# Kernel tuning notes

Measured on AMD Instinct MI355X. Metric: run time of the kernel, lower is better.

The kernel has to match this reference:

```python
import jax, jax.numpy as jnp
import numpy as np

LOOKBACK = 512
T = 131072
FEES = 0.00025


def setup_inputs() -> dict:
    key = jax.random.key(0)
    k1, k2, k3, k4 = jax.random.split(key, 4)
    features = jax.random.normal(k1, (T,), dtype=jnp.float32)
    # gross per-step asset returns near 1.0 (hourly price relatives)
    asset_returns = 1.0 + 0.01 * jax.random.normal(k2, (T,), dtype=jnp.float32)
    theta = jax.random.uniform(k3, (LOOKBACK + 2,), dtype=jnp.float32)  # torch.rand init
    p_init = jax.random.uniform(k4, (LOOKBACK - 1,), dtype=jnp.float32)  # the lookback-1 seed positions
    return {"features": features, "asset_returns": asset_returns, "theta": theta, "p_init": p_init}


def _positions(features, theta, p_init):
    lb = theta.shape[0] - 2
    n_steps = features.shape[0] - lb + 1
    # all sliding windows features[t-lb:t], t = lb..T  -> [n_steps, lb]
    idx = jnp.arange(n_steps)[:, None] + jnp.arange(lb)[None, :]
    win = features[idx]
    wmean = win.mean(axis=1, keepdims=True)
    wstd = jnp.std(win, axis=1, ddof=1, keepdims=True)  # torch.std is unbiased
    win_norm = (win - wmean) / wstd

    # running stats over ALL positions so far (growing list in the original)
    n0 = jnp.asarray(p_init.shape[0], dtype=jnp.float32)
    state0 = (n0, p_init.sum(), jnp.sum(p_init * p_init), p_init[-1])

    one = jnp.ones((1,), dtype=features.dtype)

    def step(state, w):
        n, s, ss, p_last = state
        mean = s / n
        std = jnp.sqrt((ss - n * mean * mean) / (n - 1.0))
        last_norm = (p_last - mean) / std
        xt = jnp.concatenate([w, last_norm[None], one])  # [lb+2]
        xt = (xt - xt.mean()) / jnp.std(xt, ddof=1)
        p_new = jax.nn.sigmoid(jnp.dot(theta, xt))
        return (n + 1.0, s + p_new, ss + p_new * p_new, p_new), p_new

    _, p_seq = jax.lax.scan(step, state0, win_norm)
    return jnp.concatenate([p_init, p_seq])  # length T


def _bot_returns(P, asset_returns, fees):
    inv0 = P[0]
    cash0 = 1.0 - inv0

    def step(state, rp):
        inv, cash = state
        r, p = rp
        inv = inv * r
        pv = inv + cash
        delta = pv * p - inv  # desired - current investment
        inv = inv + jnp.where(delta > 0, delta * (1.0 - fees), delta)
        cash = cash + jnp.where(delta > 0, -delta, -delta * (1.0 - fees))
        return (inv, cash), inv + cash

    _, pv_tail = jax.lax.scan(step, (inv0, cash0), (asset_returns[1:], P[1:]))
    pv = jnp.concatenate([jnp.ones((1,), dtype=pv_tail.dtype), pv_tail])  # length T
    ratios = pv[1:] / pv[:-1]
    return jnp.concatenate([jnp.ones((1,), dtype=ratios.dtype), ratios])


def reference(features, asset_returns, theta, p_init):
    P = _positions(features, theta, p_init)
    return _bot_returns(P, asset_returns, FEES)
```

## Files before the change

### kernel.cpp

```cpp
#include <hip/hip_runtime.h>
#include <math.h>

#define T_TOTAL 131072
#define LB      512
#define NSTEPS  130561
#define NPAD    130564
#define OMF     0.99975f
#define KC     -1.4426950408889634f

#define OFF_E    0
#define OFF_P0   (NPAD)
#define OFF_P    (2*NPAD)
#define OFF_BS   (2*NPAD + T_TOTAL)
#define OFF_BSS  (OFF_BS + 1024)
#define OFF_CP   (OFF_BSS + 1024)

static __device__ __forceinline__ float fast_rcp(float x) {
#if __has_builtin(__builtin_amdgcn_rcpf)
    return __builtin_amdgcn_rcpf(x);
#else
    return 1.0f / x;
#endif
}
static __device__ __forceinline__ float fast_rsq(float x) {
#if __has_builtin(__builtin_amdgcn_rsqf)
    return __builtin_amdgcn_rsqf(x);
#else
    return 1.0f / sqrtf(x);
#endif
}
static __device__ __forceinline__ float fast_exp2(float x) {
#if __has_builtin(__builtin_amdgcn_exp2f)
    return __builtin_amdgcn_exp2f(x);
#else
    return exp2f(x);
#endif
}

__global__ __launch_bounds__(256) void precompute_kernel(
    const float* __restrict__ features,
    const float* __restrict__ theta,
    const float* __restrict__ p_init,
    float* __restrict__ e_out,
    float* __restrict__ p0_out,
    float* __restrict__ P,
    float* __restrict__ bs,
    float* __restrict__ bss,
    float* __restrict__ cpool)
{
    __shared__ float f_lds[1536];
    __shared__ float th_lds[512];
    const int tid = threadIdx.x;
    const int b   = blockIdx.x;
    const int base = b * 1024;

    {
        const float4* fg = (const float4*)features;
        float4* f4s = (float4*)f_lds;
        int g0 = b * 256 + tid; g0 = g0 > 32767 ? 32767 : g0;
        f4s[tid] = fg[g0];
        if (tid < 128) {
            int g1 = b * 256 + 256 + tid; g1 = g1 > 32767 ? 32767 : g1;
            f4s[256 + tid] = fg[g1];
        }
        const float4* tg = (const float4*)theta;
        float4* t4s = (float4*)th_lds;
        if (tid >= 128 && tid < 256) t4s[tid - 128] = tg[tid - 128];
    }
    if (b == 0) {
        P[tid] = p_init[tid < 511 ? tid : 510];
        if (tid + 256 < 511) P[tid + 256] = p_init[tid + 256];
    }
    __syncthreads();

    const float4* f4 = (const float4*)f_lds;
    const float4* t4 = (const float4*)th_lds;

    float d0 = 0.f, d1 = 0.f, d2 = 0.f, d3 = 0.f;
    float fsum0 = 0.f, fss0 = 0.f, thsum = 0.f;
    float4 a = f4[tid];
    const float a00 = a.x, a01 = a.y, a02 = a.z;
#pragma unroll 4
    for (int j = 0; j < 128; ++j) {
        float4 bb = f4[tid + j + 1];
        float4 th = t4[j];
        thsum += (th.x + th.y) + (th.z + th.w);
        d0 = fmaf(th.x, a.x, d0); d0 = fmaf(th.y, a.y, d0);
        d0 = fmaf(th.z, a.z, d0); d0 = fmaf(th.w, a.w, d0);
        d1 = fmaf(th.x, a.y, d1); d1 = fmaf(th.y, a.z, d1);
        d1 = fmaf(th.z, a.w, d1); d1 = fmaf(th.w, bb.x, d1);
        d2 = fmaf(th.x, a.z, d2); d2 = fmaf(th.y, a.w, d2);
        d2 = fmaf(th.z, bb.x, d2); d2 = fmaf(th.w, bb.y, d2);
        d3 = fmaf(th.x, a.w, d3); d3 = fmaf(th.y, bb.x, d3);
        d3 = fmaf(th.z, bb.y, d3); d3 = fmaf(th.w, bb.z, d3);
        fsum0 += (a.x + a.y) + (a.z + a.w);
        fss0 = fmaf(a.x, a.x, fss0); fss0 = fmaf(a.y, a.y, fss0);
        fss0 = fmaf(a.z, a.z, fss0); fss0 = fmaf(a.w, a.w, fss0);
        a = bb;
    }
    const float b00 = a.x, b01 = a.y, b02 = a.z;
    const float fsum1 = fsum0 - a00 + b00;
    const float fsum2 = fsum1 - a01 + b01;
    const float fsum3 = fsum2 - a02 + b02;
    float fss1 = fss0 - a00 * a00; fss1 = fmaf(b00, b00, fss1);
    float fss2 = fss1 - a01 * a01; fss2 = fmaf(b01, b01, fss2);
    float fss3 = fss2 - a02 * a02; fss3 = fmaf(b02, b02, fss3);

    const float th512 = theta[512];
    const float th513 = theta[513];
    const float sall  = thsum + th512 + th513;
    const float A_    = (512.0f - 1.0f / 514.0f) / 513.0f;
    const float rsqA  = fast_rsq(A_);
    const float cE    = th513 - sall * (1.0f / 514.0f);
    if (b == 0 && tid == 0) cpool[0] = KC * (th512 - sall * (1.0f / 514.0f));

    float ez[4], pv[4];
    const float fs_[4]  = { fsum0, fsum1, fsum2, fsum3 };
    const float fq_[4]  = { fss0,  fss1,  fss2,  fss3  };
    const float dd_[4]  = { d0, d1, d2, d3 };
#pragma unroll
    for (int c = 0; c < 4; ++c) {
        float m    = fs_[c] * (1.0f / 512.0f);
        float varw = (fq_[c] - fs_[c] * m) * (1.0f / 511.0f);
        float dn   = (dd_[c] - m * thsum) * fast_rsq(varw);
        float E    = dn + cE;
        ez[c] = KC * E;
        pv[c] = fast_rcp(1.0f + fast_exp2(ez[c] * rsqA));
    }

    const int t4i = base + 4 * tid;
    if (t4i + 3 < NSTEPS) {
        ((float4*)e_out)[b * 256 + tid]  = make_float4(ez[0], ez[1], ez[2], ez[3]);
        ((float4*)p0_out)[b * 256 + tid] = make_float4(pv[0], pv[1], pv[2], pv[3]);
    } else {
#pragma unroll
        for (int c = 0; c < 4; ++c)
            if (t4i + c < NSTEPS) { e_out[t4i + c] = ez[c]; p0_out[t4i + c] = pv[c]; }
    }

    float c1 = 0.f, c2 = 0.f;
#pragma unroll
    for (int c = 0; c < 4; ++c) {
        float p = (t4i + c < NSTEPS) ? pv[c] : 0.f;
        c1 += p; c2 = fmaf(p, p, c2);
    }
#pragma unroll
    for (int dlt = 16; dlt; dlt >>= 1) {
        c1 += __shfl_down(c1, dlt, 64);
        c2 += __shfl_down(c2, dlt, 64);
    }
    if ((tid & 31) == 0) {
        int idx = b * 8 + (tid >> 5);
        bs[idx] = c1; bss[idx] = c2;
    }
}

__global__ __launch_bounds__(64) void pos_kernel(
    const float* __restrict__ p_init,
    const float* __restrict__ e,
    const float* __restrict__ p0,
    const float* __restrict__ bs,
    const float* __restrict__ bss,
    const float* __restrict__ cpool,
    float* __restrict__ P)
{
    const int l = threadIdx.x;
    const int b = blockIdx.x;
    const int g = b * 64 + l;

    float sa = 0.f, qa = 0.f;
    for (int j = l; j < 511; j += 64) { float v = p_init[j]; sa += v; qa = fmaf(v, v, qa); }
#pragma unroll
    for (int dlt = 32; dlt; dlt >>= 1) { sa += __shfl_xor(sa, dlt, 64); qa += __shfl_xor(qa, dlt, 64); }

    float ba = 0.f, ca = 0.f;
    for (int j = l; j < b * 64; j += 64) { ba += bs[j]; ca += bss[j]; }
#pragma unroll
    for (int dlt = 32; dlt; dlt >>= 1) { ba += __shfl_xor(ba, dlt, 64); ca += __shfl_xor(ca, dlt, 64); }

    float vb = (g < 1021) ? bs[g] : 0.f;
    float vc = (g < 1021) ? bss[g] : 0.f;
    float ib = vb, ic = vc;
#pragma unroll
    for (int dlt = 1; dlt < 64; dlt <<= 1) {
        float ub = __shfl_up(ib, dlt, 64);
        float uc = __shfl_up(ic, dlt, 64);
        if (l >= dlt) { ib += ub; ic += uc; }
    }
    float s  = sa + ba + (ib - vb);
    float ss = qa + ca + (ic - vc);

    if (g >= 1021) return;

    const float Gp = cpool[0];
    const float A_ = (512.0f - 1.0f / 514.0f) / 513.0f;
    const float B_ = (1.0f - 1.0f / 514.0f) / 513.0f;
    const float C_ = -2.0f / (514.0f * 513.0f);

    const int k0   = g * 128;
    const int kend = (k0 + 128 < NSTEPS) ? k0 + 128 : NSTEPS;
    const int kw   = (g == 0) ? 0 : k0 - 16;

    float plast = (g == 0) ? p_init[510] : p0[k0 - 17];
    float nf    = 511.0f + (float)k0;
    float rnm1  = fast_rcp(nf - 1.0f);

    const float mean_f = s * fast_rcp(nf);
    const float rv_f   = fast_rsq(fmaf(-s, mean_f, ss) * rnm1);

    const float4* e4 = (const float4*)(e + kw);
    const int maxi = (NPAD / 4 - 1) - (kw >> 2);

    float4 eb0[4], eb1[4];
#define LDB(DST, T) { \
    int i0 = 4 * (T); \
    DST[0] = e4[(i0 + 0) < maxi ? (i0 + 0) : maxi]; \
    DST[1] = e4[(i0 + 1) < maxi ? (i0 + 1) : maxi]; \
    DST[2] = e4[(i0 + 2) < maxi ? (i0 + 2) : maxi]; \
    DST[3] = e4[(i0 + 3) < maxi ? (i0 + 3) : maxi]; }

#define STEPF(EK, I) { \
    float rn   = fast_rcp(nf); \
    float mean = s * rn; \
    float varp = fmaf(-s, mean, ss) * rnm1; \
    float rv   = fast_rsq(varp); \
    float u    = (plast - mean) * rv; \
    float vx   = fmaf(u, fmaf(B_, u, C_), A_); \
    float r2   = fast_rsq(vx); \
    float z    = fmaf(u, Gp, (EK)) * r2; \
    float w    = fast_exp2(z); \
    float pnew = fast_rcp(1.0f + w); \
    s += pnew; ss = fmaf(pnew, pnew, ss); plast = pnew; \
    rnm1 = rn; nf += 1.0f; \
    int k = kw + (I); \
    if (k < kend) P[511 + k] = pnew; }

#define STEPW(EK) { \
    float u    = (plast - mean_f) * rv_f; \
    float vx   = fmaf(u, fmaf(B_, u, C_), A_); \
    float r2   = fast_rsq(vx); \
    float z    = fmaf(u, Gp, (EK)) * r2; \
    float w    = fast_exp2(z); \
    plast = fast_rcp(1.0f + w); }

#define FULLB(EB, IB) { \
    STEPF(EB[0].x, IB + 0);  STEPF(EB[0].y, IB + 1);  STEPF(EB[0].z, IB + 2);  STEPF(EB[0].w, IB + 3); \
    STEPF(EB[1].x, IB + 4);  STEPF(EB[1].y, IB + 5);  STEPF(EB[1].z, IB + 6);  STEPF(EB[1].w, IB + 7); \
    STEPF(EB[2].x, IB + 8);  STEPF(EB[2].y, IB + 9);  STEPF(EB[2].z, IB + 10); STEPF(EB[2].w, IB + 11); \
    STEPF(EB[3].x, IB + 12); STEPF(EB[3].y, IB + 13); STEPF(EB[3].z, IB + 14); STEPF(EB[3].w, IB + 15); }

#define WARMB(EB) { \
    STEPW(EB[0].x); STEPW(EB[0].y); STEPW(EB[0].z); STEPW(EB[0].w); \
    STEPW(EB[1].x); STEPW(EB[1].y); STEPW(EB[1].z); STEPW(EB[1].w); \
    STEPW(EB[2].x); STEPW(EB[2].y); STEPW(EB[2].z); STEPW(EB[2].w); \
    STEPW(EB[3].x); STEPW(EB[3].y); STEPW(EB[3].z); STEPW(EB[3].w); }

    LDB(eb0, 0); LDB(eb1, 1);
    if (g == 0) { FULLB(eb0, 0); } else { WARMB(eb0); }
    LDB(eb0, 2); FULLB(eb1, 16);
    LDB(eb1, 3); FULLB(eb0, 32);
    LDB(eb0, 4); FULLB(eb1, 48);
    LDB(eb1, 5); FULLB(eb0, 64);
    LDB(eb0, 6); FULLB(eb1, 80);
    LDB(eb1, 7); FULLB(eb0, 96);
    LDB(eb0, 8); FULLB(eb1, 112);
    FULLB(eb0, 128);
#undef LDB
#undef STEPF
#undef STEPW
#undef FULLB
#undef WARMB
}

__global__ __launch_bounds__(64) void port_kernel(
    const float* __restrict__ ar,
    const float* __restrict__ Pp,
    float* __restrict__ out)
{
    const int l = threadIdx.x;
    const int b = blockIdx.x;
    const int g = b * 64 + l;

    const int t0   = (g == 0) ? 1 : g * 64;
    const int tend = (t0 + 64 < T_TOTAL) ? t0 + 64 : T_TOTAL;
    const int tw   = (g == 0) ? 0 : t0 - 16;

    float x = Pp[(g == 0) ? 0 : (tw - 1)];
    float inv = x, cash = 1.0f - x, pvprev = 1.0f;
    if (g == 0) out[0] = 1.0f;

    const float4* P4 = (const float4*)(Pp + tw);
    const float4* A4 = (const float4*)(ar + tw);

    float4 pb0[4], ab0[4], pb1[4], ab1[4];
#define LDC(PD, AD, T) { \
    int i0 = 4 * (T); \
    PD[0] = P4[i0 + 0]; PD[1] = P4[i0 + 1]; PD[2] = P4[i0 + 2]; PD[3] = P4[i0 + 3]; \
    AD[0] = A4[i0 + 0]; AD[1] = A4[i0 + 1]; AD[2] = A4[i0 + 2]; AD[3] = A4[i0 + 3]; }

#define CSTEP(RR, PPV, I) { \
    int t = tw + (I); \
    float invn  = inv * (RR); \
    float pv    = invn + cash; \
    float delta = fmaf(pv, (PPV), -invn); \
    float dfee  = delta * OMF; \
    bool  pos   = delta > 0.0f; \
    float inv2  = invn + (pos ? dfee : delta); \
    float cash2 = cash - (pos ? delta : dfee); \
    float pvn   = inv2 + cash2; \
    if (t >= 1) { \
        if (t >= t0 && t < tend) out[t] = pvn * fast_rcp(pvprev); \
        inv = inv2; cash = cash2; pvprev = pvn; \
    } }

#define CBATCH(PB, AB, IB) { \
    CSTEP(AB[0].x, PB[0].x, IB + 0);  CSTEP(AB[0].y, PB[0].y, IB + 1); \
    CSTEP(AB[0].z, PB[0].z, IB + 2);  CSTEP(AB[0].w, PB[0].w, IB + 3); \
    CSTEP(AB[1].x, PB[1].x, IB + 4);  CSTEP(AB[1].y, PB[1].y, IB + 5); \
    CSTEP(AB[1].z, PB[1].z, IB + 6);  CSTEP(AB[1].w, PB[1].w, IB + 7); \
    CSTEP(AB[2].x, PB[2].x, IB + 8);  CSTEP(AB[2].y, PB[2].y, IB + 9); \
    CSTEP(AB[2].z, PB[2].z, IB + 10); CSTEP(AB[2].w, PB[2].w, IB + 11); \
    CSTEP(AB[3].x, PB[3].x, IB + 12); CSTEP(AB[3].y, PB[3].y, IB + 13); \
    CSTEP(AB[3].z, PB[3].z, IB + 14); CSTEP(AB[3].w, PB[3].w, IB + 15); }

    LDC(pb0, ab0, 0); LDC(pb1, ab1, 1);
    CBATCH(pb0, ab0, 0);  LDC(pb0, ab0, 2);
    CBATCH(pb1, ab1, 16); LDC(pb1, ab1, 3);
    CBATCH(pb0, ab0, 32); LDC(pb0, ab0, 4);
    CBATCH(pb1, ab1, 48);
    CBATCH(pb0, ab0, 64);
#undef LDC
#undef CSTEP
#undef CBATCH
}

extern "C" void kernel_launch(void* const* d_in, const int* in_sizes, int n_in,
                              void* d_out, int out_size, void* d_ws, size_t ws_size,
                              hipStream_t stream) {
    const float* features      = (const float*)d_in[0];
    const float* asset_returns = (const float*)d_in[1];
    const float* theta         = (const float*)d_in[2];
    const float* p_init        = (const float*)d_in[3];
    float* out = (float*)d_out;
    float* ws  = (float*)d_ws;

    float* e_arr = ws + OFF_E;
    float* p0    = ws + OFF_P0;
    float* P     = ws + OFF_P;
    float* bs    = ws + OFF_BS;
    float* bss   = ws + OFF_BSS;
    float* cpool = ws + OFF_CP;

    precompute_kernel<<<128, 256, 0, stream>>>(features, theta, p_init,
                                               e_arr, p0, P, bs, bss, cpool);
    pos_kernel<<<16, 64, 0, stream>>>(p_init, e_arr, p0, bs, bss, cpool, P);
    port_kernel<<<32, 64, 0, stream>>>(asset_returns, P, out);
}
```

Baseline: 99.43 us.

## Fuse three kernels into one persistent kernel with grid barriers, halve chunk sizes

Merges the precompute, position-scan and portfolio-scan kernels into one 128-block launch separated by atomic-counter grid barriers, plus a tiny init kernel that zeroes the counters. This removes two kernel-launch gaps. The sequential chunks are halved (64-step position chunks with 8-step warm-up, 32-step portfolio chunks with 8-step warm-up), so more threads run shorter serial chains. Partial sums are now taken per 16 lanes to match the smaller chunks. The costs are barrier spin overhead, an extra launch for the counter reset, and shorter warm-up windows that could reduce accuracy.

```diff
diff --git a/kernel.cpp b/kernel.cpp
--- a/kernel.cpp
+++ b/kernel.cpp
@@ -12,8 +12,9 @@
 #define OFF_P0   (NPAD)
 #define OFF_P    (2*NPAD)
 #define OFF_BS   (2*NPAD + T_TOTAL)
-#define OFF_BSS  (OFF_BS + 1024)
-#define OFF_CP   (OFF_BSS + 1024)
+#define OFF_BSS  (OFF_BS + 2048)
+#define OFF_CP   (OFF_BSS + 2048)
+#define OFF_CTR  (OFF_CP + 16)
 
 static __device__ __forceinline__ float fast_rcp(float x) {
 #if __has_builtin(__builtin_amdgcn_rcpf)
@@ -37,189 +38,205 @@
 #endif
 }
 
-__global__ __launch_bounds__(256) void precompute_kernel(
+static __device__ __forceinline__ void grid_barrier(unsigned* ctr, unsigned nblk) {
+    __syncthreads();
+    if (threadIdx.x == 0) {
+        __threadfence();
+        __hip_atomic_fetch_add(ctr, 1u, __ATOMIC_ACQ_REL, __HIP_MEMORY_SCOPE_AGENT);
+        while (__hip_atomic_load(ctr, __ATOMIC_ACQUIRE, __HIP_MEMORY_SCOPE_AGENT) < nblk) {
+            __builtin_amdgcn_s_sleep(8);
+        }
+        __threadfence();
+    }
+    __syncthreads();
+}
+
+__global__ __launch_bounds__(64) void init_kernel(unsigned* ctr) {
+    ctr[threadIdx.x] = 0u;
+}
+
+__global__ __launch_bounds__(256) void fused_kernel(
     const float* __restrict__ features,
+    const float* __restrict__ asset_returns,
     const float* __restrict__ theta,
     const float* __restrict__ p_init,
-    float* __restrict__ e_out,
-    float* __restrict__ p0_out,
-    float* __restrict__ P,
-    float* __restrict__ bs,
-    float* __restrict__ bss,
-    float* __restrict__ cpool)
+    float* __restrict__ out,
+    float* __restrict__ ws)
 {
+    float* e_out = ws + OFF_E;
+    float* p0    = ws + OFF_P0;
+    float* P     = ws + OFF_P;
+    float* bs    = ws + OFF_BS;
+    float* bss   = ws + OFF_BSS;
+    float* cpool = ws + OFF_CP;
+    unsigned* ctr = (unsigned*)(ws + OFF_CTR);
+
     __shared__ float f_lds[1536];
     __shared__ float th_lds[512];
     const int tid = threadIdx.x;
     const int b   = blockIdx.x;
-    const int base = b * 1024;
 
     {
-        const float4* fg = (const float4*)features;
-        float4* f4s = (float4*)f_lds;
-        int g0 = b * 256 + tid; g0 = g0 > 32767 ? 32767 : g0;
-        f4s[tid] = fg[g0];
-        if (tid < 128) {
-            int g1 = b * 256 + 256 + tid; g1 = g1 > 32767 ? 32767 : g1;
-            f4s[256 + tid] = fg[g1];
-        }
-        const float4* tg = (const float4*)theta;
-        float4* t4s = (float4*)th_lds;
-        if (tid >= 128 && tid < 256) t4s[tid - 128] = tg[tid - 128];
+        const int base = b * 1024;
+        {
+            const float4* fg = (const float4*)features;
+            float4* f4s = (float4*)f_lds;
+            int g0 = b * 256 + tid; g0 = g0 > 32767 ? 32767 : g0;
+            f4s[tid] = fg[g0];
+            if (tid < 128) {
+                int g1 = b * 256 + 256 + tid; g1 = g1 > 32767 ? 32767 : g1;
+                f4s[256 + tid] = fg[g1];
+            }
+            const float4* tg = (const float4*)theta;
+            float4* t4s = (float4*)th_lds;
+            if (tid >= 128 && tid < 256) t4s[tid - 128] = tg[tid - 128];
+        }
+        if (b == 0) {
+            P[tid] = p_init[tid < 511 ? tid : 510];
+            if (tid + 256 < 511) P[tid + 256] = p_init[tid + 256];
+        }
+        __syncthreads();
+
+        float thsum = 0.f;
+        {
+            int l6 = tid & 63;
+#pragma unroll
+            for (int j = 0; j < 8; ++j) thsum += th_lds[l6 + 64 * j];
+#pragma unroll
+            for (int d = 32; d; d >>= 1) thsum += __shfl_xor(thsum, d, 64);
+        }
+
+        const float4* f4 = (const float4*)f_lds;
+        const float4* t4 = (const float4*)th_lds;
+
+        float d0 = 0.f, d1 = 0.f, d2 = 0.f, d3 = 0.f;
+        float fsum0 = 0.f, fss0 = 0.f;
+        float4 a = f4[tid];
+        const float a00 = a.x, a01 = a.y, a02 = a.z;
+#pragma unroll 4
+        for (int j = 0; j < 128; ++j) {
+            float4 bb = f4[tid + j + 1];
+            float4 th = t4[j];
+            d0 = fmaf(th.x, a.x, d0); d0 = fmaf(th.y, a.y, d0);
+            d0 = fmaf(th.z, a.z, d0); d0 = fmaf(th.w, a.w, d0);
+            d1 = fmaf(th.x, a.y, d1); d1 = fmaf(th.y, a.z, d1);
+            d1 = fmaf(th.z, a.w, d1); d1 = fmaf(th.w, bb.x, d1);
+            d2 = fmaf(th.x, a.z, d2); d2 = fmaf(th.y, a.w, d2);
+            d2 = fmaf(th.z, bb.x, d2); d2 = fmaf(th.w, bb.y, d2);
+            d3 = fmaf(th.x, a.w, d3); d3 = fmaf(th.y, bb.x, d3);
+            d3 = fmaf(th.z, bb.y, d3); d3 = fmaf(th.w, bb.z, d3);
+            fsum0 += (a.x + a.y) + (a.z + a.w);
+            fss0 = fmaf(a.x, a.x, fss0); fss0 = fmaf(a.y, a.y, fss0);
+            fss0 = fmaf(a.z, a.z, fss0); fss0 = fmaf(a.w, a.w, fss0);
+            a = bb;
+        }
+        const float b00 = a.x, b01 = a.y, b02 = a.z;
+        const float fsum1 = fsum0 - a00 + b00;
+        const float fsum2 = fsum1 - a01 + b01;
+        const float fsum3 = fsum2 - a02 + b02;
+        float fss1 = fss0 - a00 * a00; fss1 = fmaf(b00, b00, fss1);
+        float fss2 = fss1 - a01 * a01; fss2 = fmaf(b01, b01, fss2);
+        float fss3 = fss2 - a02 * a02; fss3 = fmaf(b02, b02, fss3);
+
+        const float th512 = theta[512];
+        const float th513 = theta[513];
+        const float sall  = thsum + th512 + th513;
+        const float A_    = (512.0f - 1.0f / 514.0f) / 513.0f;
+        const float rsqA  = fast_rsq(A_);
+        const float cE    = th513 - sall * (1.0f / 514.0f);
+        if (b == 0 && tid == 0) cpool[0] = KC * (th512 - sall * (1.0f / 514.0f));
+
+        float ez[4], pv[4];
+        const float fs_[4] = { fsum0, fsum1, fsum2, fsum3 };
+        const float fq_[4] = { fss0,  fss1,  fss2,  fss3  };
+        const float dd_[4] = { d0, d1, d2, d3 };
+#pragma unroll
+        for (int c = 0; c < 4; ++c) {
+            float m    = fs_[c] * (1.0f / 512.0f);
+            float varw = (fq_[c] - fs_[c] * m) * (1.0f / 511.0f);
+            float dn   = (dd_[c] - m * thsum) * fast_rsq(varw);
+            ez[c] = KC * (dn + cE);
+            pv[c] = fast_rcp(1.0f + fast_exp2(ez[c] * rsqA));
+        }
+
+        const int t4i = base + 4 * tid;
+        if (t4i + 3 < NSTEPS) {
+            ((float4*)e_out)[b * 256 + tid] = make_float4(ez[0], ez[1], ez[2], ez[3]);
+            ((float4*)p0)[b * 256 + tid]    = make_float4(pv[0], pv[1], pv[2], pv[3]);
+        } else {
+#pragma unroll
+            for (int c = 0; c < 4; ++c)
+                if (t4i + c < NSTEPS) { e_out[t4i + c] = ez[c]; p0[t4i + c] = pv[c]; }
+        }
+
+        float c1 = 0.f, c2 = 0.f;
+#pragma unroll
+        for (int c = 0; c < 4; ++c) {
+            float p = (t4i + c < NSTEPS) ? pv[c] : 0.f;
+            c1 += p; c2 = fmaf(p, p, c2);
+        }
+#pragma unroll
+        for (int d = 8; d; d >>= 1) {
+            c1 += __shfl_down(c1, d, 16);
+            c2 += __shfl_down(c2, d, 16);
+        }
+        if ((tid & 15) == 0) {
+            int idx = b * 16 + (tid >> 4);
+            bs[idx] = c1; bss[idx] = c2;
+        }
     }
-    if (b == 0) {
-        P[tid] = p_init[tid < 511 ? tid : 510];
-        if (tid + 256 < 511) P[tid + 256] = p_init[tid + 256];
-    }
-    __syncthreads();
-
-    const float4* f4 = (const float4*)f_lds;
-    const float4* t4 = (const float4*)th_lds;
-
-    float d0 = 0.f, d1 = 0.f, d2 = 0.f, d3 = 0.f;
-    float fsum0 = 0.f, fss0 = 0.f, thsum = 0.f;
-    float4 a = f4[tid];
-    const float a00 = a.x, a01 = a.y, a02 = a.z;
-#pragma unroll 4
-    for (int j = 0; j < 128; ++j) {
-        float4 bb = f4[tid + j + 1];
-        float4 th = t4[j];
-        thsum += (th.x + th.y) + (th.z + th.w);
-        d0 = fmaf(th.x, a.x, d0); d0 = fmaf(th.y, a.y, d0);
-        d0 = fmaf(th.z, a.z, d0); d0 = fmaf(th.w, a.w, d0);
-        d1 = fmaf(th.x, a.y, d1); d1 = fmaf(th.y, a.z, d1);
-        d1 = fmaf(th.z, a.w, d1); d1 = fmaf(th.w, bb.x, d1);
-        d2 = fmaf(th.x, a.z, d2); d2 = fmaf(th.y, a.w, d2);
-        d2 = fmaf(th.z, bb.x, d2); d2 = fmaf(th.w, bb.y, d2);
-        d3 = fmaf(th.x, a.w, d3); d3 = fmaf(th.y, bb.x, d3);
-        d3 = fmaf(th.z, bb.y, d3); d3 = fmaf(th.w, bb.z, d3);
-        fsum0 += (a.x + a.y) + (a.z + a.w);
-        fss0 = fmaf(a.x, a.x, fss0); fss0 = fmaf(a.y, a.y, fss0);
-        fss0 = fmaf(a.z, a.z, fss0); fss0 = fmaf(a.w, a.w, fss0);
-        a = bb;
-    }
-    const float b00 = a.x, b01 = a.y, b02 = a.z;
-    const float fsum1 = fsum0 - a00 + b00;
-    const float fsum2 = fsum1 - a01 + b01;
-    const float fsum3 = fsum2 - a02 + b02;
-    float fss1 = fss0 - a00 * a00; fss1 = fmaf(b00, b00, fss1);
-    float fss2 = fss1 - a01 * a01; fss2 = fmaf(b01, b01, fss2);
-    float fss3 = fss2 - a02 * a02; fss3 = fmaf(b02, b02, fss3);
-
-    const float th512 = theta[512];
-    const float th513 = theta[513];
-    const float sall  = thsum + th512 + th513;
-    const float A_    = (512.0f - 1.0f / 514.0f) / 513.0f;
-    const float rsqA  = fast_rsq(A_);
-    const float cE    = th513 - sall * (1.0f / 514.0f);
-    if (b == 0 && tid == 0) cpool[0] = KC * (th512 - sall * (1.0f / 514.0f));
-
-    float ez[4], pv[4];
-    const float fs_[4]  = { fsum0, fsum1, fsum2, fsum3 };
-    const float fq_[4]  = { fss0,  fss1,  fss2,  fss3  };
-    const float dd_[4]  = { d0, d1, d2, d3 };
-#pragma unroll
-    for (int c = 0; c < 4; ++c) {
-        float m    = fs_[c] * (1.0f / 512.0f);
-        float varw = (fq_[c] - fs_[c] * m) * (1.0f / 511.0f);
-        float dn   = (dd_[c] - m * thsum) * fast_rsq(varw);
-        float E    = dn + cE;
-        ez[c] = KC * E;
-        pv[c] = fast_rcp(1.0f + fast_exp2(ez[c] * rsqA));
-    }
-
-    const int t4i = base + 4 * tid;
-    if (t4i + 3 < NSTEPS) {
-        ((float4*)e_out)[b * 256 + tid]  = make_float4(ez[0], ez[1], ez[2], ez[3]);
-        ((float4*)p0_out)[b * 256 + tid] = make_float4(pv[0], pv[1], pv[2], pv[3]);
-    } else {
-#pragma unroll
-        for (int c = 0; c < 4; ++c)
-            if (t4i + c < NSTEPS) { e_out[t4i + c] = ez[c]; p0_out[t4i + c] = pv[c]; }
-    }
-
-    float c1 = 0.f, c2 = 0.f;
-#pragma unroll
-    for (int c = 0; c < 4; ++c) {
-        float p = (t4i + c < NSTEPS) ? pv[c] : 0.f;
-        c1 += p; c2 = fmaf(p, p, c2);
-    }
-#pragma unroll
-    for (int dlt = 16; dlt; dlt >>= 1) {
-        c1 += __shfl_down(c1, dlt, 64);
-        c2 += __shfl_down(c2, dlt, 64);
-    }
-    if ((tid & 31) == 0) {
-        int idx = b * 8 + (tid >> 5);
-        bs[idx] = c1; bss[idx] = c2;
-    }
-}
-
-__global__ __launch_bounds__(64) void pos_kernel(
-    const float* __restrict__ p_init,
-    const float* __restrict__ e,
-    const float* __restrict__ p0,
-    const float* __restrict__ bs,
-    const float* __restrict__ bss,
-    const float* __restrict__ cpool,
-    float* __restrict__ P)
-{
-    const int l = threadIdx.x;
-    const int b = blockIdx.x;
-    const int g = b * 64 + l;
-
-    float sa = 0.f, qa = 0.f;
-    for (int j = l; j < 511; j += 64) { float v = p_init[j]; sa += v; qa = fmaf(v, v, qa); }
-#pragma unroll
-    for (int dlt = 32; dlt; dlt >>= 1) { sa += __shfl_xor(sa, dlt, 64); qa += __shfl_xor(qa, dlt, 64); }
-
-    float ba = 0.f, ca = 0.f;
-    for (int j = l; j < b * 64; j += 64) { ba += bs[j]; ca += bss[j]; }
-#pragma unroll
-    for (int dlt = 32; dlt; dlt >>= 1) { ba += __shfl_xor(ba, dlt, 64); ca += __shfl_xor(ca, dlt, 64); }
-
-    float vb = (g < 1021) ? bs[g] : 0.f;
-    float vc = (g < 1021) ? bss[g] : 0.f;
-    float ib = vb, ic = vc;
-#pragma unroll
-    for (int dlt = 1; dlt < 64; dlt <<= 1) {
-        float ub = __shfl_up(ib, dlt, 64);
-        float uc = __shfl_up(ic, dlt, 64);
-        if (l >= dlt) { ib += ub; ic += uc; }
-    }
-    float s  = sa + ba + (ib - vb);
-    float ss = qa + ca + (ic - vc);
-
-    if (g >= 1021) return;
-
-    const float Gp = cpool[0];
-    const float A_ = (512.0f - 1.0f / 514.0f) / 513.0f;
-    const float B_ = (1.0f - 1.0f / 514.0f) / 513.0f;
-    const float C_ = -2.0f / (514.0f * 513.0f);
-
-    const int k0   = g * 128;
-    const int kend = (k0 + 128 < NSTEPS) ? k0 + 128 : NSTEPS;
-    const int kw   = (g == 0) ? 0 : k0 - 16;
-
-    float plast = (g == 0) ? p_init[510] : p0[k0 - 17];
-    float nf    = 511.0f + (float)k0;
-    float rnm1  = fast_rcp(nf - 1.0f);
-
-    const float mean_f = s * fast_rcp(nf);
-    const float rv_f   = fast_rsq(fmaf(-s, mean_f, ss) * rnm1);
-
-    const float4* e4 = (const float4*)(e + kw);
-    const int maxi = (NPAD / 4 - 1) - (kw >> 2);
-
-    float4 eb0[4], eb1[4];
-#define LDB(DST, T) { \
-    int i0 = 4 * (T); \
-    DST[0] = e4[(i0 + 0) < maxi ? (i0 + 0) : maxi]; \
-    DST[1] = e4[(i0 + 1) < maxi ? (i0 + 1) : maxi]; \
-    DST[2] = e4[(i0 + 2) < maxi ? (i0 + 2) : maxi]; \
-    DST[3] = e4[(i0 + 3) < maxi ? (i0 + 3) : maxi]; }
-
-#define STEPF(EK, I) { \
+
+    grid_barrier(&ctr[0], 128);
+
+    if (b < 32 && tid < 64) {
+        const int l = tid;
+        const int g = b * 64 + l;
+
+        float sa = 0.f, qa = 0.f;
+        for (int j = l; j < 511; j += 64) { float v = p_init[j]; sa += v; qa = fmaf(v, v, qa); }
+#pragma unroll
+        for (int d = 32; d; d >>= 1) { sa += __shfl_xor(sa, d, 64); qa += __shfl_xor(qa, d, 64); }
+
+        float ba = 0.f, ca = 0.f;
+        for (int j = l; j < b * 64; j += 64) { ba += bs[j]; ca += bss[j]; }
+#pragma unroll
+        for (int d = 32; d; d >>= 1) { ba += __shfl_xor(ba, d, 64); ca += __shfl_xor(ca, d, 64); }
+
+        float vb = bs[g], vc = bss[g];
+        float ib = vb, ic = vc;
+#pragma unroll
+        for (int d = 1; d < 64; d <<= 1) {
+            float ub = __shfl_up(ib, d, 64);
+            float uc = __shfl_up(ic, d, 64);
+            if (l >= d) { ib += ub; ic += uc; }
+        }
+        float s  = sa + ba + (ib - vb);
+        float ss = qa + ca + (ic - vc);
+
+        if (g <= 2040) {
+            const float Gp = cpool[0];
+            const float A_ = (512.0f - 1.0f / 514.0f) / 513.0f;
+            const float B_ = (1.0f - 1.0f / 514.0f) / 513.0f;
+            const float C_ = -2.0f / (514.0f * 513.0f);
+
+            const int k0   = g * 64;
+            const int kend = (k0 + 64 < NSTEPS) ? k0 + 64 : NSTEPS;
+            const int kw   = (g == 0) ? 0 : k0 - 8;
+
+            float plast = (g == 0) ? p_init[510] : p0[k0 - 9];
+            float nf    = 511.0f + (float)k0;
+            float rnm1  = fast_rcp(nf - 1.0f);
+            const float mean_f = s * fast_rcp(nf);
+            const float rv_f   = fast_rsq(fmaf(-s, mean_f, ss) * rnm1);
+
+            const float4* e4 = (const float4*)(e_out + kw);
+            const int maxi = (NPAD / 4 - 1) - (kw >> 2);
+
+            float4 er[18];
+#pragma unroll
+            for (int i = 0; i < 18; ++i) er[i] = e4[i < maxi ? i : maxi];
+
+#define BSTEP(EK, I) { \
     float rn   = fast_rcp(nf); \
     float mean = s * rn; \
     float varp = fmaf(-s, mean, ss) * rnm1; \
@@ -234,104 +251,72 @@
     rnm1 = rn; nf += 1.0f; \
     int k = kw + (I); \
     if (k < kend) P[511 + k] = pnew; }
-
-#define STEPW(EK) { \
-    float u    = (plast - mean_f) * rv_f; \
-    float vx   = fmaf(u, fmaf(B_, u, C_), A_); \
-    float r2   = fast_rsq(vx); \
-    float z    = fmaf(u, Gp, (EK)) * r2; \
-    float w    = fast_exp2(z); \
-    plast = fast_rcp(1.0f + w); }
-
-#define FULLB(EB, IB) { \
-    STEPF(EB[0].x, IB + 0);  STEPF(EB[0].y, IB + 1);  STEPF(EB[0].z, IB + 2);  STEPF(EB[0].w, IB + 3); \
-    STEPF(EB[1].x, IB + 4);  STEPF(EB[1].y, IB + 5);  STEPF(EB[1].z, IB + 6);  STEPF(EB[1].w, IB + 7); \
-    STEPF(EB[2].x, IB + 8);  STEPF(EB[2].y, IB + 9);  STEPF(EB[2].z, IB + 10); STEPF(EB[2].w, IB + 11); \
-    STEPF(EB[3].x, IB + 12); STEPF(EB[3].y, IB + 13); STEPF(EB[3].z, IB + 14); STEPF(EB[3].w, IB + 15); }
-
-#define WARMB(EB) { \
-    STEPW(EB[0].x); STEPW(EB[0].y); STEPW(EB[0].z); STEPW(EB[0].w); \
-    STEPW(EB[1].x); STEPW(EB[1].y); STEPW(EB[1].z); STEPW(EB[1].w); \
-    STEPW(EB[2].x); STEPW(EB[2].y); STEPW(EB[2].z); STEPW(EB[2].w); \
-    STEPW(EB[3].x); STEPW(EB[3].y); STEPW(EB[3].z); STEPW(EB[3].w); }
-
-    LDB(eb0, 0); LDB(eb1, 1);
-    if (g == 0) { FULLB(eb0, 0); } else { WARMB(eb0); }
-    LDB(eb0, 2); FULLB(eb1, 16);
-    LDB(eb1, 3); FULLB(eb0, 32);
-    LDB(eb0, 4); FULLB(eb1, 48);
-    LDB(eb1, 5); FULLB(eb0, 64);
-    LDB(eb0, 6); FULLB(eb1, 80);
-    LDB(eb1, 7); FULLB(eb0, 96);
-    LDB(eb0, 8); FULLB(eb1, 112);
-    FULLB(eb0, 128);
-#undef LDB
-#undef STEPF
-#undef STEPW
-#undef FULLB
-#undef WARMB
-}
-
-__global__ __launch_bounds__(64) void port_kernel(
-    const float* __restrict__ ar,
-    const float* __restrict__ Pp,
-    float* __restrict__ out)
-{
-    const int l = threadIdx.x;
-    const int b = blockIdx.x;
-    const int g = b * 64 + l;
-
-    const int t0   = (g == 0) ? 1 : g * 64;
-    const int tend = (t0 + 64 < T_TOTAL) ? t0 + 64 : T_TOTAL;
-    const int tw   = (g == 0) ? 0 : t0 - 16;
-
-    float x = Pp[(g == 0) ? 0 : (tw - 1)];
-    float inv = x, cash = 1.0f - x, pvprev = 1.0f;
-    if (g == 0) out[0] = 1.0f;
-
-    const float4* P4 = (const float4*)(Pp + tw);
-    const float4* A4 = (const float4*)(ar + tw);
-
-    float4 pb0[4], ab0[4], pb1[4], ab1[4];
-#define LDC(PD, AD, T) { \
-    int i0 = 4 * (T); \
-    PD[0] = P4[i0 + 0]; PD[1] = P4[i0 + 1]; PD[2] = P4[i0 + 2]; PD[3] = P4[i0 + 3]; \
-    AD[0] = A4[i0 + 0]; AD[1] = A4[i0 + 1]; AD[2] = A4[i0 + 2]; AD[3] = A4[i0 + 3]; }
-
-#define CSTEP(RR, PPV, I) { \
+#define BWARM(EK) { \
+    float u  = (plast - mean_f) * rv_f; \
+    float vx = fmaf(u, fmaf(B_, u, C_), A_); \
+    float r2 = fast_rsq(vx); \
+    float z  = fmaf(u, Gp, (EK)) * r2; \
+    plast = fast_rcp(1.0f + fast_exp2(z)); }
+#define B4(Q, IB) { BSTEP(Q.x, IB+0); BSTEP(Q.y, IB+1); BSTEP(Q.z, IB+2); BSTEP(Q.w, IB+3); }
+#define W4(Q) { BWARM(Q.x); BWARM(Q.y); BWARM(Q.z); BWARM(Q.w); }
+
+            if (g == 0) { B4(er[0], 0); B4(er[1], 4); }
+            else        { W4(er[0]);    W4(er[1]);    }
+            B4(er[2],  8);  B4(er[3], 12);  B4(er[4], 16);  B4(er[5], 20);
+            B4(er[6], 24);  B4(er[7], 28);  B4(er[8], 32);  B4(er[9], 36);
+            B4(er[10],40);  B4(er[11],44);  B4(er[12],48);  B4(er[13],52);
+            B4(er[14],56);  B4(er[15],60);  B4(er[16],64);  B4(er[17],68);
+#undef BSTEP
+#undef BWARM
+#undef B4
+#undef W4
+        }
+    }
+
+    grid_barrier(&ctr[32], 128);
+
+    if (tid < 32) {
+        const int g = b * 32 + tid;
+        const int t0   = g * 32;
+        const int t0w  = (g == 0) ? 1 : t0;
+        const int tend = (t0 + 32 < T_TOTAL) ? t0 + 32 : T_TOTAL;
+        const int tw   = (g == 0) ? 0 : t0 - 8;
+
+        float x = P[(g == 0) ? 0 : (tw - 1)];
+        float inv = x, cash = 1.0f - x, pvprev = 1.0f;
+        if (g == 0) out[0] = 1.0f;
+
+        const float4* P4 = (const float4*)(P + tw);
+        const float4* A4 = (const float4*)(asset_returns + tw);
+
+        float4 pr[10], ar[10];
+#pragma unroll
+        for (int i = 0; i < 10; ++i) { pr[i] = P4[i]; ar[i] = A4[i]; }
+
+#define CST(RR, PPV, I) { \
     int t = tw + (I); \
-    float invn  = inv * (RR); \
-    float pv    = invn + cash; \
-    float delta = fmaf(pv, (PPV), -invn); \
-    float dfee  = delta * OMF; \
-    bool  pos   = delta > 0.0f; \
-    float inv2  = invn + (pos ? dfee : delta); \
-    float cash2 = cash - (pos ? delta : dfee); \
-    float pvn   = inv2 + cash2; \
     if (t >= 1) { \
-        if (t >= t0 && t < tend) out[t] = pvn * fast_rcp(pvprev); \
-        inv = inv2; cash = cash2; pvprev = pvn; \
-    } }
-
-#define CBATCH(PB, AB, IB) { \
-    CSTEP(AB[0].x, PB[0].x, IB + 0);  CSTEP(AB[0].y, PB[0].y, IB + 1); \
-    CSTEP(AB[0].z, PB[0].z, IB + 2);  CSTEP(AB[0].w, PB[0].w, IB + 3); \
-    CSTEP(AB[1].x, PB[1].x, IB + 4);  CSTEP(AB[1].y, PB[1].y, IB + 5); \
-    CSTEP(AB[1].z, PB[1].z, IB + 6);  CSTEP(AB[1].w, PB[1].w, IB + 7); \
-    CSTEP(AB[2].x, PB[2].x, IB + 8);  CSTEP(AB[2].y, PB[2].y, IB + 9); \
-    CSTEP(AB[2].z, PB[2].z, IB + 10); CSTEP(AB[2].w, PB[2].w, IB + 11); \
-    CSTEP(AB[3].x, PB[3].x, IB + 12); CSTEP(AB[3].y, PB[3].y, IB + 13); \
-    CSTEP(AB[3].z, PB[3].z, IB + 14); CSTEP(AB[3].w, PB[3].w, IB + 15); }
-
-    LDC(pb0, ab0, 0); LDC(pb1, ab1, 1);
-    CBATCH(pb0, ab0, 0);  LDC(pb0, ab0, 2);
-    CBATCH(pb1, ab1, 16); LDC(pb1, ab1, 3);
-    CBATCH(pb0, ab0, 32); LDC(pb0, ab0, 4);
-    CBATCH(pb1, ab1, 48);
-    CBATCH(pb0, ab0, 64);
-#undef LDC
-#undef CSTEP
-#undef CBATCH
+        float invn  = inv * (RR); \
+        float pv    = invn + cash; \
+        float delta = fmaf(pv, (PPV), -invn); \
+        float dfee  = delta * OMF; \
+        bool  pos   = delta > 0.0f; \
+        inv  = invn + (pos ? dfee : delta); \
+        cash = cash - (pos ? delta : dfee); \
+        float pvn = inv + cash; \
+        if (t >= t0w && t < tend) out[t] = pvn * fast_rcp(pvprev); \
+        pvprev = pvn; } }
+#define C4(PQ, AQ, IB) { CST(AQ.x, PQ.x, IB+0); CST(AQ.y, PQ.y, IB+1); \
+                         CST(AQ.z, PQ.z, IB+2); CST(AQ.w, PQ.w, IB+3); }
+
+        C4(pr[0], ar[0], 0);   C4(pr[1], ar[1], 4);
+        C4(pr[2], ar[2], 8);   C4(pr[3], ar[3], 12);
+        C4(pr[4], ar[4], 16);  C4(pr[5], ar[5], 20);
+        C4(pr[6], ar[6], 24);  C4(pr[7], ar[7], 28);
+        C4(pr[8], ar[8], 32);  C4(pr[9], ar[9], 36);
+#undef CST
+#undef C4
+    }
 }
 
 extern "C" void kernel_launch(void* const* d_in, const int* in_sizes, int n_in,
@@ -343,16 +328,8 @@
     const float* p_init        = (const float*)d_in[3];
     float* out = (float*)d_out;
     float* ws  = (float*)d_ws;
-
-    float* e_arr = ws + OFF_E;
-    float* p0    = ws + OFF_P0;
-    float* P     = ws + OFF_P;
-    float* bs    = ws + OFF_BS;
-    float* bss   = ws + OFF_BSS;
-    float* cpool = ws + OFF_CP;
-
-    precompute_kernel<<<128, 256, 0, stream>>>(features, theta, p_init,
-                                               e_arr, p0, P, bs, bss, cpool);
-    pos_kernel<<<16, 64, 0, stream>>>(p_init, e_arr, p0, bs, bss, cpool, P);
-    port_kernel<<<32, 64, 0, stream>>>(asset_returns, P, out);
-}
+    unsigned* ctr = (unsigned*)(ws + OFF_CTR);
+
+    init_kernel<<<1, 64, 0, stream>>>(ctr);
+    fused_kernel<<<128, 256, 0, stream>>>(features, asset_returns, theta, p_init, out, ws);
+}
```

New measurement: 132.4 us. 1.33x slower.
